# Performance work log

Hardware: AMD Instinct MI355X
Metric: run time of the kernel (lower is better)

## Reference

```python
import jax, jax.numpy as jnp
import numpy as np

NUM_UPDATES = 4

def setup_inputs() -> dict:
    key = jax.random.key(0)
    ks = jax.random.split(key, 14)
    N, E = 1024, 64
    s1, sE, s2E = 1.0, 1.0 / np.sqrt(E), 1.0 / np.sqrt(2 * E)
    inp = {
        'nodes_features': jax.random.normal(ks[0], (1, N), jnp.float32),
        'nodes_cost': jax.random.uniform(ks[1], (N, N), jnp.float32),
        'W1': jax.random.normal(ks[2], (E, 1), jnp.float32) * s1,
        'b1': jax.random.normal(ks[3], (E,), jnp.float32) * s1,
        'W2': jax.random.normal(ks[4], (E, E), jnp.float32) * sE,
        'b2': jax.random.normal(ks[5], (E,), jnp.float32) * sE,
        'W4': jax.random.normal(ks[6], (E, 1), jnp.float32) * s1,
        'b4': jax.random.normal(ks[7], (E,), jnp.float32) * s1,
        'W5': jax.random.normal(ks[8], (1, 2 * E), jnp.float32) * s2E,
        'b5': jax.random.normal(ks[9], (1,), jnp.float32) * s2E,
        'W6': jax.random.normal(ks[10], (E, E), jnp.float32) * sE,
        'b6': jax.random.normal(ks[11], (E,), jnp.float32) * sE,
        'W7': jax.random.normal(ks[12], (E, E), jnp.float32) * sE,
        'b7': jax.random.normal(ks[13], (E,), jnp.float32) * sE,
    }
    return inp

def reference(nodes_features, nodes_cost, W1, b1, W2, b2, W4, b4, W5, b5, W6, b6, W7, b7):
    x = nodes_features.T                      # (N, 1) per-node feature
    N = x.shape[0]
    E = W1.shape[0]
    # vector1 per node (constant across updates): linear1(x_v)
    V1 = x @ W1.T + b1                        # (N, E)
    # vector3 per node (constant across updates):
    # sum_i relu(cost[i, v] * w4 + b4)  -> elementwise over (N, N, E), memory-bound
    w4 = W4[:, 0]                             # (E,)
    V3 = jax.nn.relu(nodes_cost[:, :, None] * w4[None, None, :] + b4).sum(axis=0)  # (N, E)
    base = V1 + V3                            # (N, E)

    # Synchronous updates: new_emb[v] = relu(base[v] + linear2(old_emb.sum(0)))
    def step(emb, _):
        v2 = emb.sum(axis=0) @ W2.T + b2      # (E,) shared across nodes
        return jax.nn.relu(base + v2[None, :]), None

    emb0 = jnp.zeros((N, E), dtype=x.dtype)
    emb, _ = jax.lax.scan(step, emb0, None, length=NUM_UPDATES)

    # Q(v) = linear5(relu(concat(linear6(sum emb), linear7(emb[v]))))
    s = emb.sum(axis=0)                       # (E,)
    h1 = s @ W6.T + b6                        # (E,) shared
    h2 = emb @ W7.T + b7                      # (N, E)
    h = jax.nn.relu(jnp.concatenate([jnp.broadcast_to(h1, (N, E)), h2], axis=1))  # (N, 2E)
    q = h @ W5.T + b5                         # (N, 1)
    return q
```

## Files before the change

kernel.cpp:

```cpp
#include <hip/hip_runtime.h>

#define NN 1024
#define EE 64

__global__ __launch_bounds__(256) void k1a_part(
    const float* __restrict__ cost,
    const float* __restrict__ w4, const float* __restrict__ b4,
    float* __restrict__ partial)
{
    const int it = blockIdx.x;
    const int jc = blockIdx.y;
    const int jspan = NN / gridDim.y;
    const int tid = threadIdx.x;
    const int il = tid & 31;
    const int eg = tid >> 5;
    const int i = it * 32 + il;
    const int j0 = jc * jspan;

    float w4v[8], b4v[8];
#pragma unroll
    for (int ee = 0; ee < 8; ++ee) {
        int e = eg * 8 + ee;
        w4v[ee] = w4[e];
        b4v[ee] = b4[e];
    }

    float acc[8];
#pragma unroll
    for (int ee = 0; ee < 8; ++ee) acc[ee] = 0.f;

    const float* cp = cost + (size_t)j0 * NN + i;
#pragma unroll 8
    for (int jj = 0; jj < jspan; ++jj) {
        float cv = cp[(size_t)jj * NN];
#pragma unroll
        for (int ee = 0; ee < 8; ++ee)
            acc[ee] += fmaxf(fmaf(cv, w4v[ee], b4v[ee]), 0.f);
    }

    float* dst = partial + ((size_t)jc * NN + i) * EE + eg * 8;
    float4 v0 = make_float4(acc[0], acc[1], acc[2], acc[3]);
    float4 v1 = make_float4(acc[4], acc[5], acc[6], acc[7]);
    *(float4*)(dst)     = v0;
    *(float4*)(dst + 4) = v1;
}

__global__ __launch_bounds__(256) void k1b_reduce(
    const float* __restrict__ nf,
    const float* __restrict__ W1, const float* __restrict__ b1,
    const float* __restrict__ partial, int nparts,
    float* __restrict__ base)
{
    const int idx = blockIdx.x * 256 + threadIdx.x;
    const int i = idx >> 6;
    const int e = idx & 63;
    float s0 = fmaf(nf[i], W1[e], b1[e]);
    float s1 = 0.f;
#pragma unroll 4
    for (int p = 0; p + 1 < nparts; p += 2) {
        s0 += partial[(size_t)p * (NN * EE) + idx];
        s1 += partial[(size_t)(p + 1) * (NN * EE) + idx];
    }
    if (nparts & 1) s0 += partial[(size_t)(nparts - 1) * (NN * EE) + idx];
    base[idx] = s0 + s1;
}

__global__ __launch_bounds__(1024) void k2_scan(
    const float* __restrict__ base,
    const float* __restrict__ W2, const float* __restrict__ b2,
    const float* __restrict__ W5,
    const float* __restrict__ W6, const float* __restrict__ b6,
    float* __restrict__ v2out, float* __restrict__ Cout)
{
    __shared__ float W2L[64 * 65];
    __shared__ float sP[1024];
    __shared__ float sS[64];
    __shared__ float sV[64];
    const int tid = threadIdx.x;
    const int c = tid & 63;
    const int g = tid >> 6;

#pragma unroll
    for (int m = tid; m < 4096; m += 1024)
        W2L[(m >> 6) * 65 + (m & 63)] = W2[m];

    float bl[64];
#pragma unroll
    for (int rr = 0; rr < 64; ++rr)
        bl[rr] = base[(size_t)(g * 64 + rr) * EE + c];

    if (tid < 64) sS[c] = 0.f;
    __syncthreads();

    for (int t = 0; t < 4; ++t) {
        if (tid < 64) {
            float v = b2[c];
#pragma unroll
            for (int k = 0; k < 64; ++k) v = fmaf(W2L[c * 65 + k], sS[k], v);
            sV[c] = v;
        }
        __syncthreads();
        float v2c = sV[c];
        float acc = 0.f;
#pragma unroll
        for (int rr = 0; rr < 64; ++rr) acc += fmaxf(bl[rr] + v2c, 0.f);
        sP[tid] = acc;
        __syncthreads();
        if (tid < 64) {
            float s = 0.f;
#pragma unroll
            for (int gg = 0; gg < 16; ++gg) s += sP[gg * 64 + c];
            sS[c] = s;
        }
        __syncthreads();
    }

    if (tid < 64) {
        float h = b6[c];
        for (int k = 0; k < 64; ++k) h = fmaf(W6[c * 64 + k], sS[k], h);
        float p = fmaxf(h, 0.f) * W5[c];
#pragma unroll
        for (int off = 32; off > 0; off >>= 1) p += __shfl_down(p, off, 64);
        v2out[c] = sV[c];
        if (tid == 0) Cout[0] = p;
    }
}

__global__ __launch_bounds__(256) void k3_out(
    const float* __restrict__ base,
    const float* __restrict__ W7, const float* __restrict__ b7,
    const float* __restrict__ W5, const float* __restrict__ b5,
    const float* __restrict__ v2, const float* __restrict__ Cin,
    float* __restrict__ q)
{
    __shared__ float W7L[64 * 65];
    __shared__ float embL[4 * 64];
    const int tid = threadIdx.x;
    const int lane = tid & 63;
    const int rl = tid >> 6;
    const int i = blockIdx.x * 4 + rl;

    for (int m = tid; m < 4096; m += 256)
        W7L[(m >> 6) * 65 + (m & 63)] = W7[m];

    float ev = fmaxf(base[(size_t)i * EE + lane] + v2[lane], 0.f);
    embL[rl * 64 + lane] = ev;
    __syncthreads();

    float h = b7[lane];
#pragma unroll
    for (int k = 0; k < 64; ++k)
        h = fmaf(embL[rl * 64 + k], W7L[lane * 65 + k], h);
    float p = fmaxf(h, 0.f) * W5[64 + lane];
#pragma unroll
    for (int off = 32; off > 0; off >>= 1) p += __shfl_down(p, off, 64);
    if (lane == 0) q[i] = p + Cin[0] + b5[0];
}

extern "C" void kernel_launch(void* const* d_in, const int* in_sizes, int n_in,
                              void* d_out, int out_size, void* d_ws, size_t ws_size,
                              hipStream_t stream)
{
    (void)in_sizes; (void)n_in; (void)out_size;
    const float* nf   = (const float*)d_in[0];
    const float* cost = (const float*)d_in[1];
    const float* W1   = (const float*)d_in[2];
    const float* b1   = (const float*)d_in[3];
    const float* W2   = (const float*)d_in[4];
    const float* b2   = (const float*)d_in[5];
    const float* w4   = (const float*)d_in[6];
    const float* b4   = (const float*)d_in[7];
    const float* W5   = (const float*)d_in[8];
    const float* b5   = (const float*)d_in[9];
    const float* W6   = (const float*)d_in[10];
    const float* b6   = (const float*)d_in[11];
    const float* W7   = (const float*)d_in[12];
    const float* b7   = (const float*)d_in[13];
    float* q    = (float*)d_out;

    float* base = (float*)d_ws;
    float* v2o  = base + (size_t)NN * EE;
    float* Co   = v2o + EE;
    float* part = Co + 1;

    size_t fixed = ((size_t)NN * EE + EE + 1) * sizeof(float);
    size_t per_part = (size_t)NN * EE * sizeof(float);
    int nparts = 16;
    while (nparts > 1 && fixed + (size_t)nparts * per_part > ws_size) nparts >>= 1;

    dim3 g1(32, nparts);
    k1a_part<<<g1, 256, 0, stream>>>(cost, w4, b4, part);
    k1b_reduce<<<256, 256, 0, stream>>>(nf, W1, b1, part, nparts, base);
    k2_scan<<<1, 1024, 0, stream>>>(base, W2, b2, W5, W6, b6, v2o, Co);
    k3_out<<<256, 256, 0, stream>>>(base, W7, b7, W5, b5, v2o, Co, q);
}
```

Baseline: 32.80 us.

## Fuse all four stages into one cooperative kernel with grid syncs

Replaces the four separate launches (partial ReLU-sum, reduce, serial scan, output projection) with a single cooperative kernel of 256 blocks of 1024 threads, using grid.sync between phases. Block 0 alone runs the 4-step scan while the other blocks wait at the barrier. The first phase's work split also changes to 64 nodes by 4 features per thread. It aims to remove launch gaps between dependent kernels, but adds grid-wide barrier costs and requires all 256 large blocks to be co-resident. The old multi-kernel path is kept as a fallback when the workspace is too small.

```diff
diff --git a/kernel.cpp b/kernel.cpp
--- a/kernel.cpp
+++ b/kernel.cpp
@@ -1,7 +1,146 @@
 #include <hip/hip_runtime.h>
+#include <hip/hip_cooperative_groups.h>
+
+namespace cg = cooperative_groups;
 
 #define NN 1024
 #define EE 64
+#define NPARTS 16
+
+__global__ __launch_bounds__(1024) void s2v_fused(
+    const float* __restrict__ nf, const float* __restrict__ cost,
+    const float* __restrict__ W1, const float* __restrict__ b1,
+    const float* __restrict__ W2, const float* __restrict__ b2,
+    const float* __restrict__ w4, const float* __restrict__ b4,
+    const float* __restrict__ W5, const float* __restrict__ b5,
+    const float* __restrict__ W6, const float* __restrict__ b6,
+    const float* __restrict__ W7, const float* __restrict__ b7,
+    float* __restrict__ partial, float* __restrict__ base,
+    float* __restrict__ v2o, float* __restrict__ Co,
+    float* __restrict__ q)
+{
+    cg::grid_group grid = cg::this_grid();
+    const int gid = blockIdx.x;
+    const int tid = threadIdx.x;
+
+    __shared__ float WL[64 * 65];
+    __shared__ float sP[1024];
+    __shared__ float sS[64];
+    __shared__ float sV[64];
+    __shared__ float embL[4 * 64];
+
+    {
+        const int it = gid & 15;
+        const int jc = gid >> 4;
+        const int il = tid & 63;
+        const int eg = tid >> 6;
+        const int i  = it * 64 + il;
+
+        float w4v[4], b4v[4];
+#pragma unroll
+        for (int ee = 0; ee < 4; ++ee) {
+            w4v[ee] = w4[eg * 4 + ee];
+            b4v[ee] = b4[eg * 4 + ee];
+        }
+        float a0 = 0.f, a1 = 0.f, a2 = 0.f, a3 = 0.f;
+        const float* cp = cost + (size_t)jc * 64 * NN + i;
+#pragma unroll 8
+        for (int jj = 0; jj < 64; ++jj) {
+            float cv = cp[(size_t)jj * NN];
+            a0 += fmaxf(fmaf(cv, w4v[0], b4v[0]), 0.f);
+            a1 += fmaxf(fmaf(cv, w4v[1], b4v[1]), 0.f);
+            a2 += fmaxf(fmaf(cv, w4v[2], b4v[2]), 0.f);
+            a3 += fmaxf(fmaf(cv, w4v[3], b4v[3]), 0.f);
+        }
+        float4 v = make_float4(a0, a1, a2, a3);
+        *(float4*)(partial + ((size_t)jc * NN + i) * EE + eg * 4) = v;
+    }
+    grid.sync();
+
+    if (tid < 256) {
+        const int idx = gid * 256 + tid;
+        const int i = idx >> 6, e = idx & 63;
+        float s = fmaf(nf[i], W1[e], b1[e]);
+#pragma unroll
+        for (int p = 0; p < NPARTS; ++p)
+            s += partial[(size_t)p * (NN * EE) + idx];
+        base[idx] = s;
+    }
+    grid.sync();
+
+    if (gid == 0) {
+        const int c = tid & 63;
+        const int g = tid >> 6;
+#pragma unroll
+        for (int m = tid; m < 4096; m += 1024)
+            WL[(m >> 6) * 65 + (m & 63)] = W2[m];
+        float bl[64];
+#pragma unroll
+        for (int rr = 0; rr < 64; ++rr)
+            bl[rr] = base[(size_t)(g * 64 + rr) * EE + c];
+        if (tid < 64) sS[c] = 0.f;
+        __syncthreads();
+
+        for (int t = 0; t < 4; ++t) {
+            if (tid < 64) {
+                float v = b2[c];
+#pragma unroll
+                for (int k = 0; k < 64; ++k) v = fmaf(WL[c * 65 + k], sS[k], v);
+                sV[c] = v;
+            }
+            __syncthreads();
+            float v2c = sV[c];
+            float acc = 0.f;
+#pragma unroll
+            for (int rr = 0; rr < 64; ++rr) acc += fmaxf(bl[rr] + v2c, 0.f);
+            sP[tid] = acc;
+            __syncthreads();
+            if (tid < 64) {
+                float s = 0.f;
+#pragma unroll
+                for (int gg = 0; gg < 16; ++gg) s += sP[gg * 64 + c];
+                sS[c] = s;
+            }
+            __syncthreads();
+        }
+
+        if (tid < 64) {
+            float h = b6[c];
+            for (int k = 0; k < 64; ++k) h = fmaf(W6[c * 64 + k], sS[k], h);
+            float p = fmaxf(h, 0.f) * W5[c];
+#pragma unroll
+            for (int off = 32; off > 0; off >>= 1) p += __shfl_down(p, off, 64);
+            v2o[c] = sV[c];
+            if (tid == 0) Co[0] = p;
+        }
+    }
+    grid.sync();
+
+    {
+#pragma unroll
+        for (int m = tid; m < 4096; m += 1024)
+            WL[(m >> 6) * 65 + (m & 63)] = W7[m];
+        const int lane = tid & 63;
+        const int w = tid >> 6;
+        if (w < 4) {
+            const int i = gid * 4 + w;
+            embL[w * 64 + lane] =
+                fmaxf(base[(size_t)i * EE + lane] + v2o[lane], 0.f);
+        }
+        __syncthreads();
+        if (w < 4) {
+            const int i = gid * 4 + w;
+            float h = b7[lane];
+#pragma unroll
+            for (int k = 0; k < 64; ++k)
+                h = fmaf(embL[w * 64 + k], WL[lane * 65 + k], h);
+            float p = fmaxf(h, 0.f) * W5[64 + lane];
+#pragma unroll
+            for (int off = 32; off > 0; off >>= 1) p += __shfl_down(p, off, 64);
+            if (lane == 0) q[i] = p + Co[0] + b5[0];
+        }
+    }
+}
 
 __global__ __launch_bounds__(256) void k1a_part(
     const float* __restrict__ cost,
@@ -20,11 +159,9 @@
     float w4v[8], b4v[8];
 #pragma unroll
     for (int ee = 0; ee < 8; ++ee) {
-        int e = eg * 8 + ee;
-        w4v[ee] = w4[e];
-        b4v[ee] = b4[e];
-    }
-
+        w4v[ee] = w4[eg * 8 + ee];
+        b4v[ee] = b4[eg * 8 + ee];
+    }
     float acc[8];
 #pragma unroll
     for (int ee = 0; ee < 8; ++ee) acc[ee] = 0.f;
@@ -37,12 +174,9 @@
         for (int ee = 0; ee < 8; ++ee)
             acc[ee] += fmaxf(fmaf(cv, w4v[ee], b4v[ee]), 0.f);
     }
-
     float* dst = partial + ((size_t)jc * NN + i) * EE + eg * 8;
-    float4 v0 = make_float4(acc[0], acc[1], acc[2], acc[3]);
-    float4 v1 = make_float4(acc[4], acc[5], acc[6], acc[7]);
-    *(float4*)(dst)     = v0;
-    *(float4*)(dst + 4) = v1;
+    *(float4*)(dst)     = make_float4(acc[0], acc[1], acc[2], acc[3]);
+    *(float4*)(dst + 4) = make_float4(acc[4], acc[5], acc[6], acc[7]);
 }
 
 __global__ __launch_bounds__(256) void k1b_reduce(
@@ -54,15 +188,10 @@
     const int idx = blockIdx.x * 256 + threadIdx.x;
     const int i = idx >> 6;
     const int e = idx & 63;
-    float s0 = fmaf(nf[i], W1[e], b1[e]);
-    float s1 = 0.f;
-#pragma unroll 4
-    for (int p = 0; p + 1 < nparts; p += 2) {
-        s0 += partial[(size_t)p * (NN * EE) + idx];
-        s1 += partial[(size_t)(p + 1) * (NN * EE) + idx];
-    }
-    if (nparts & 1) s0 += partial[(size_t)(nparts - 1) * (NN * EE) + idx];
-    base[idx] = s0 + s1;
+    float s = fmaf(nf[i], W1[e], b1[e]);
+    for (int p = 0; p < nparts; ++p)
+        s += partial[(size_t)p * (NN * EE) + idx];
+    base[idx] = s;
 }
 
 __global__ __launch_bounds__(1024) void k2_scan(
@@ -79,19 +208,15 @@
     const int tid = threadIdx.x;
     const int c = tid & 63;
     const int g = tid >> 6;
-
 #pragma unroll
     for (int m = tid; m < 4096; m += 1024)
         W2L[(m >> 6) * 65 + (m & 63)] = W2[m];
-
     float bl[64];
 #pragma unroll
     for (int rr = 0; rr < 64; ++rr)
         bl[rr] = base[(size_t)(g * 64 + rr) * EE + c];
-
     if (tid < 64) sS[c] = 0.f;
     __syncthreads();
-
     for (int t = 0; t < 4; ++t) {
         if (tid < 64) {
             float v = b2[c];
@@ -114,7 +239,6 @@
         }
         __syncthreads();
     }
-
     if (tid < 64) {
         float h = b6[c];
         for (int k = 0; k < 64; ++k) h = fmaf(W6[c * 64 + k], sS[k], h);
@@ -139,14 +263,11 @@
     const int lane = tid & 63;
     const int rl = tid >> 6;
     const int i = blockIdx.x * 4 + rl;
-
     for (int m = tid; m < 4096; m += 256)
         W7L[(m >> 6) * 65 + (m & 63)] = W7[m];
-
     float ev = fmaxf(base[(size_t)i * EE + lane] + v2[lane], 0.f);
     embL[rl * 64 + lane] = ev;
     __syncthreads();
-
     float h = b7[lane];
 #pragma unroll
     for (int k = 0; k < 64; ++k)
@@ -176,21 +297,37 @@
     const float* b6   = (const float*)d_in[11];
     const float* W7   = (const float*)d_in[12];
     const float* b7   = (const float*)d_in[13];
-    float* q    = (float*)d_out;
-
-    float* base = (float*)d_ws;
+    float* q = (float*)d_out;
+
+    float* part = (float*)d_ws;
+    float* base = part + (size_t)NPARTS * NN * EE;
     float* v2o  = base + (size_t)NN * EE;
     float* Co   = v2o + EE;
-    float* part = Co + 1;
-
-    size_t fixed = ((size_t)NN * EE + EE + 1) * sizeof(float);
-    size_t per_part = (size_t)NN * EE * sizeof(float);
-    int nparts = 16;
-    while (nparts > 1 && fixed + (size_t)nparts * per_part > ws_size) nparts >>= 1;
-
-    dim3 g1(32, nparts);
-    k1a_part<<<g1, 256, 0, stream>>>(cost, w4, b4, part);
-    k1b_reduce<<<256, 256, 0, stream>>>(nf, W1, b1, part, nparts, base);
-    k2_scan<<<1, 1024, 0, stream>>>(base, W2, b2, W5, W6, b6, v2o, Co);
-    k3_out<<<256, 256, 0, stream>>>(base, W7, b7, W5, b5, v2o, Co, q);
-}
+
+    size_t need = ((size_t)NPARTS * NN * EE + (size_t)NN * EE + EE + 1) * sizeof(float);
+
+    if (ws_size >= need) {
+        void* args[] = {
+            (void*)&nf, (void*)&cost, (void*)&W1, (void*)&b1, (void*)&W2,
+            (void*)&b2, (void*)&w4, (void*)&b4, (void*)&W5, (void*)&b5,
+            (void*)&W6, (void*)&b6, (void*)&W7, (void*)&b7,
+            (void*)&part, (void*)&base, (void*)&v2o, (void*)&Co, (void*)&q
+        };
+        hipLaunchCooperativeKernel((void*)s2v_fused, dim3(256), dim3(1024),
+                                   args, 0, stream);
+    } else {
+        float* fb_base = (float*)d_ws;
+        float* fb_v2o  = fb_base + (size_t)NN * EE;
+        float* fb_Co   = fb_v2o + EE;
+        float* fb_part = fb_Co + 1;
+        size_t fixed = ((size_t)NN * EE + EE + 1) * sizeof(float);
+        size_t per_part = (size_t)NN * EE * sizeof(float);
+        int nparts = 16;
+        while (nparts > 1 && fixed + (size_t)nparts * per_part > ws_size) nparts >>= 1;
+        dim3 g1(32, nparts);
+        k1a_part<<<g1, 256, 0, stream>>>(cost, w4, b4, fb_part);
+        k1b_reduce<<<256, 256, 0, stream>>>(nf, W1, b1, fb_part, nparts, fb_base);
+        k2_scan<<<1, 1024, 0, stream>>>(fb_base, W2, b2, W5, W6, b6, fb_v2o, fb_Co);
+        k3_out<<<256, 256, 0, stream>>>(fb_base, W7, b7, W5, b5, fb_v2o, fb_Co, q);
+    }
+}
```

After: 124.7 us. 280% more time.

## Fuse scan and output kernels by recomputing the scan in every block

Applied to the files above, without the earlier changes.

The single-block scan kernel and the output kernel are merged into one launch of 64 blocks of 1024 threads. Each block redundantly recomputes the 4-step embedding-sum scan and the shared h1 term, then handles 16 output rows. This removes one kernel launch and the global round-trip of v2 and the scalar, at the cost of 64 times the redundant scan work and more shared memory per block. The per-thread reduction is also split into four accumulators to shorten the dependency chain.

```diff
diff --git a/kernel.cpp b/kernel.cpp
--- a/kernel.cpp
+++ b/kernel.cpp
@@ -20,11 +20,9 @@
     float w4v[8], b4v[8];
 #pragma unroll
     for (int ee = 0; ee < 8; ++ee) {
-        int e = eg * 8 + ee;
-        w4v[ee] = w4[e];
-        b4v[ee] = b4[e];
+        w4v[ee] = w4[eg * 8 + ee];
+        b4v[ee] = b4[eg * 8 + ee];
     }
-
     float acc[8];
 #pragma unroll
     for (int ee = 0; ee < 8; ++ee) acc[ee] = 0.f;
@@ -37,12 +35,9 @@
         for (int ee = 0; ee < 8; ++ee)
             acc[ee] += fmaxf(fmaf(cv, w4v[ee], b4v[ee]), 0.f);
     }
-
     float* dst = partial + ((size_t)jc * NN + i) * EE + eg * 8;
-    float4 v0 = make_float4(acc[0], acc[1], acc[2], acc[3]);
-    float4 v1 = make_float4(acc[4], acc[5], acc[6], acc[7]);
-    *(float4*)(dst)     = v0;
-    *(float4*)(dst + 4) = v1;
+    *(float4*)(dst)     = make_float4(acc[0], acc[1], acc[2], acc[3]);
+    *(float4*)(dst + 4) = make_float4(acc[4], acc[5], acc[6], acc[7]);
 }
 
 __global__ __launch_bounds__(256) void k1b_reduce(
@@ -65,24 +60,31 @@
     base[idx] = s0 + s1;
 }
 
-__global__ __launch_bounds__(1024) void k2_scan(
+__global__ __launch_bounds__(1024) void k23_fused(
     const float* __restrict__ base,
     const float* __restrict__ W2, const float* __restrict__ b2,
-    const float* __restrict__ W5,
+    const float* __restrict__ W5, const float* __restrict__ b5,
     const float* __restrict__ W6, const float* __restrict__ b6,
-    float* __restrict__ v2out, float* __restrict__ Cout)
+    const float* __restrict__ W7, const float* __restrict__ b7,
+    float* __restrict__ q)
 {
     __shared__ float W2L[64 * 65];
+    __shared__ float W7L[64 * 65];
     __shared__ float sP[1024];
     __shared__ float sS[64];
     __shared__ float sV[64];
+    __shared__ float embL[16 * 64];
+    __shared__ float sC;
+
     const int tid = threadIdx.x;
     const int c = tid & 63;
     const int g = tid >> 6;
 
 #pragma unroll
-    for (int m = tid; m < 4096; m += 1024)
+    for (int m = tid; m < 4096; m += 1024) {
         W2L[(m >> 6) * 65 + (m & 63)] = W2[m];
+        W7L[(m >> 6) * 65 + (m & 63)] = W7[m];
+    }
 
     float bl[64];
 #pragma unroll
@@ -101,10 +103,15 @@
         }
         __syncthreads();
         float v2c = sV[c];
-        float acc = 0.f;
+        float a0 = 0.f, a1 = 0.f, a2 = 0.f, a3 = 0.f;
 #pragma unroll
-        for (int rr = 0; rr < 64; ++rr) acc += fmaxf(bl[rr] + v2c, 0.f);
-        sP[tid] = acc;
+        for (int rr = 0; rr < 64; rr += 4) {
+            a0 += fmaxf(bl[rr]     + v2c, 0.f);
+            a1 += fmaxf(bl[rr + 1] + v2c, 0.f);
+            a2 += fmaxf(bl[rr + 2] + v2c, 0.f);
+            a3 += fmaxf(bl[rr + 3] + v2c, 0.f);
+        }
+        sP[tid] = (a0 + a1) + (a2 + a3);
         __syncthreads();
         if (tid < 64) {
             float s = 0.f;
@@ -117,44 +124,26 @@
 
     if (tid < 64) {
         float h = b6[c];
+#pragma unroll
         for (int k = 0; k < 64; ++k) h = fmaf(W6[c * 64 + k], sS[k], h);
         float p = fmaxf(h, 0.f) * W5[c];
 #pragma unroll
         for (int off = 32; off > 0; off >>= 1) p += __shfl_down(p, off, 64);
-        v2out[c] = sV[c];
-        if (tid == 0) Cout[0] = p;
+        if (tid == 0) sC = p;
     }
-}
 
-__global__ __launch_bounds__(256) void k3_out(
-    const float* __restrict__ base,
-    const float* __restrict__ W7, const float* __restrict__ b7,
-    const float* __restrict__ W5, const float* __restrict__ b5,
-    const float* __restrict__ v2, const float* __restrict__ Cin,
-    float* __restrict__ q)
-{
-    __shared__ float W7L[64 * 65];
-    __shared__ float embL[4 * 64];
-    const int tid = threadIdx.x;
-    const int lane = tid & 63;
-    const int rl = tid >> 6;
-    const int i = blockIdx.x * 4 + rl;
-
-    for (int m = tid; m < 4096; m += 256)
-        W7L[(m >> 6) * 65 + (m & 63)] = W7[m];
-
-    float ev = fmaxf(base[(size_t)i * EE + lane] + v2[lane], 0.f);
-    embL[rl * 64 + lane] = ev;
+    const int i = blockIdx.x * 16 + g;
+    embL[g * 64 + c] = fmaxf(base[(size_t)i * EE + c] + sV[c], 0.f);
     __syncthreads();
 
-    float h = b7[lane];
+    float h = b7[c];
 #pragma unroll
     for (int k = 0; k < 64; ++k)
-        h = fmaf(embL[rl * 64 + k], W7L[lane * 65 + k], h);
-    float p = fmaxf(h, 0.f) * W5[64 + lane];
+        h = fmaf(embL[g * 64 + k], W7L[c * 65 + k], h);
+    float p = fmaxf(h, 0.f) * W5[64 + c];
 #pragma unroll
     for (int off = 32; off > 0; off >>= 1) p += __shfl_down(p, off, 64);
-    if (lane == 0) q[i] = p + Cin[0] + b5[0];
+    if (c == 0) q[i] = p + sC + b5[0];
 }
 
 extern "C" void kernel_launch(void* const* d_in, const int* in_sizes, int n_in,
@@ -176,14 +165,12 @@
     const float* b6   = (const float*)d_in[11];
     const float* W7   = (const float*)d_in[12];
     const float* b7   = (const float*)d_in[13];
-    float* q    = (float*)d_out;
+    float* q = (float*)d_out;
 
     float* base = (float*)d_ws;
-    float* v2o  = base + (size_t)NN * EE;
-    float* Co   = v2o + EE;
-    float* part = Co + 1;
+    float* part = base + (size_t)NN * EE;
 
-    size_t fixed = ((size_t)NN * EE + EE + 1) * sizeof(float);
+    size_t fixed = (size_t)NN * EE * sizeof(float);
     size_t per_part = (size_t)NN * EE * sizeof(float);
     int nparts = 16;
     while (nparts > 1 && fixed + (size_t)nparts * per_part > ws_size) nparts >>= 1;
@@ -191,6 +178,5 @@
     dim3 g1(32, nparts);
     k1a_part<<<g1, 256, 0, stream>>>(cost, w4, b4, part);
     k1b_reduce<<<256, 256, 0, stream>>>(nf, W1, b1, part, nparts, base);
-    k2_scan<<<1, 1024, 0, stream>>>(base, W2, b2, W5, W6, b6, v2o, Co);
-    k3_out<<<256, 256, 0, stream>>>(base, W7, b7, W5, b5, v2o, Co, q);
+    k23_fused<<<64, 1024, 0, stream>>>(base, W2, b2, W5, b5, W6, b6, W7, b7, q);
 }
```

Measured after the change: 32.47 us. About the same (-1.0%).
